# Performance work log

Measured on AMD Instinct MI355X. Metric: run time of the kernel, lower is better.

Reference implementation:

```python
import jax, jax.numpy as jnp
import numpy as np

B, N_ENT, D = 8, 50000, 64
ATTN = 64
TOTAL_REL = 401
E = 1000000


def setup_inputs() -> dict:
    key = jax.random.key(0)
    ks = jax.random.split(key, 16)
    inp = {
        "query": jax.random.normal(ks[0], (B, D), jnp.float32),
        "hidden": jax.random.normal(ks[1], (B, N_ENT, D), jnp.float32),
        # params
        "Ws": jax.random.normal(ks[2], (ATTN, D), jnp.float32) / np.sqrt(D),
        "Wr": jax.random.normal(ks[3], (ATTN, D), jnp.float32) / np.sqrt(D),
        "Wqr_w": jax.random.normal(ks[4], (ATTN, D), jnp.float32) / np.sqrt(D),
        "Wqr_b": jnp.zeros((ATTN,), jnp.float32),
        "Wattn": jax.random.normal(ks[5], (1, ATTN), jnp.float32) / np.sqrt(ATTN),
        "rela_embed": jax.random.normal(ks[6], (TOTAL_REL, D), jnp.float32),
        "mlp_w1": jax.random.normal(ks[7], (D, D), jnp.float32) / np.sqrt(D),
        "mlp_b1": jnp.zeros((D,), jnp.float32),
        "mlp_w2": jax.random.normal(ks[8], (D, D), jnp.float32) / np.sqrt(D),
        "mlp_b2": jnp.zeros((D,), jnp.float32),
        # edge list columns
        "id_bat": jax.random.randint(ks[9], (E,), 0, B),
        "id_sub": jax.random.randint(ks[10], (E,), 0, B * N_ENT),
        "id_rel": jax.random.randint(ks[11], (E,), 0, TOTAL_REL),
        "id_obj": jax.random.randint(ks[12], (E,), 0, B * N_ENT),
    }
    return inp


def reference(query, hidden, Ws, Wr, Wqr_w, Wqr_b, Wattn, rela_embed,
              mlp_w1, mlp_b1, mlp_w2, mlp_b2,
              id_bat, id_sub, id_rel, id_obj):
    b, n_ent, d = hidden.shape
    all_h = hidden.reshape(b * n_ent, d)
    # gathers
    m_head = all_h[id_sub]            # [E, D]
    m_rela = rela_embed[id_rel]       # [E, D]
    m_quer = query[id_bat]            # [E, D]
    # distmult message
    mess = m_head * m_rela
    # attention gate: sigmoid(W_attn(relu(Ws h + Wr r + Wqr q + b)))
    pre = jax.nn.relu(m_head @ Ws.T + m_rela @ Wr.T + m_quer @ Wqr_w.T + Wqr_b)
    alpha = jax.nn.sigmoid(pre @ Wattn.T)   # [E, 1]
    message = mess * alpha
    # scatter-sum aggregation to [B*n_ent, D]
    agg = jax.ops.segment_sum(message, id_obj, num_segments=b * n_ent)
    # unique-index masked MLP update: MLP applied only to nodes that received
    # messages; untouched rows stay exactly zero (as in the torch original)
    touched = jnp.zeros((b * n_ent,), bool).at[id_obj].set(True)
    upd = jax.nn.relu((agg @ mlp_w1.T + mlp_b1) @ mlp_w2.T + mlp_b2)
    new_hidden = jnp.where(touched[:, None], upd, jnp.zeros((), upd.dtype))
    return new_hidden.reshape(b, n_ent, d)
```

## Files before the change

kernel.cpp:

```cpp
#include <hip/hip_runtime.h>
#include <math.h>

#define COUNT_BLOCKS 256

__device__ __forceinline__ void proj_rows(
    const float* __restrict__ x, const float* __restrict__ W,
    const float* __restrict__ bias, float* __restrict__ y,
    int base, int nrows, float* __restrict__ smem)
{
    int t = threadIdx.x;
    float4* sm4 = (float4*)smem;
    for (int i = t; i < 1024; i += 256) sm4[i] = ((const float4*)W)[i];
    __syncthreads();

    int tid = t & 127;
    int c0  = (t >> 7) * 32;
    int r0  = base + tid;
    bool v[4];
#pragma unroll
    for (int k = 0; k < 4; ++k) v[k] = (r0 + k * 128) < nrows;
    if (!v[0]) return;

    float acc[4][32];
#pragma unroll
    for (int k = 0; k < 4; ++k)
#pragma unroll
        for (int a = 0; a < 32; ++a) acc[k][a] = bias ? bias[c0 + a] : 0.f;

    for (int d4 = 0; d4 < 16; ++d4) {
        float4 xv[4];
#pragma unroll
        for (int k = 0; k < 4; ++k)
            xv[k] = v[k] ? *(const float4*)(x + (size_t)(r0 + k * 128) * 64 + d4 * 4)
                         : make_float4(0.f, 0.f, 0.f, 0.f);
#pragma unroll
        for (int a = 0; a < 32; ++a) {
            float4 w4 = sm4[(c0 + a) * 16 + d4];
#pragma unroll
            for (int k = 0; k < 4; ++k) {
                acc[k][a] = fmaf(xv[k].x, w4.x, acc[k][a]);
                acc[k][a] = fmaf(xv[k].y, w4.y, acc[k][a]);
                acc[k][a] = fmaf(xv[k].z, w4.z, acc[k][a]);
                acc[k][a] = fmaf(xv[k].w, w4.w, acc[k][a]);
            }
        }
    }
#pragma unroll
    for (int k = 0; k < 4; ++k) if (v[k]) {
        float* yr = y + (size_t)(r0 + k * 128) * 64 + c0;
#pragma unroll
        for (int a4 = 0; a4 < 8; ++a4)
            *(float4*)(yr + a4 * 4) = make_float4(acc[k][a4*4+0], acc[k][a4*4+1],
                                                  acc[k][a4*4+2], acc[k][a4*4+3]);
    }
}

__device__ __forceinline__ void combine_device(
    const float* __restrict__ w1, const float* __restrict__ b1,
    const float* __restrict__ w2, const float* __restrict__ b2,
    float* __restrict__ WcT, float* __restrict__ bc, float* __restrict__ smem)
{
    int t = threadIdx.x;
    float4* sm4 = (float4*)smem;
    for (int i = t; i < 1024; i += 256) sm4[i] = ((const float4*)w1)[i];
    __syncthreads();
    int j = t >> 2, k0 = (t & 3) * 16;
    for (int k = k0; k < k0 + 16; ++k) {
        float a = 0.f;
        for (int tt = 0; tt < 64; ++tt)
            a = fmaf(w2[j * 64 + tt], smem[tt * 64 + k], a);
        WcT[k * 64 + j] = a;
    }
    if ((t & 3) == 0) {
        float a = b2[j];
        for (int tt = 0; tt < 64; ++tt) a = fmaf(w2[j * 64 + tt], b1[tt], a);
        bc[j] = a;
    }
}

__device__ __forceinline__ void count_device(
    const int* __restrict__ id_obj, int* __restrict__ counts, int E, int cb)
{
    int e = cb * 256 + (int)threadIdx.x;
    int stride = COUNT_BLOCKS * 256;
    for (; e < E; e += stride) atomicAdd(&counts[id_obj[e]], 1);
}

__global__ __launch_bounds__(256, 1) void prepare(
    const float* __restrict__ hidden, const float* __restrict__ Ws,
    float* __restrict__ hs, int NN, int pbNN,
    const float* __restrict__ rela, const float* __restrict__ Wr,
    float* __restrict__ rr, int NR,
    const float* __restrict__ query, const float* __restrict__ Wqr_w,
    const float* __restrict__ Wqr_b, float* __restrict__ qq, int B,
    const float* __restrict__ w1, const float* __restrict__ b1,
    const float* __restrict__ w2, const float* __restrict__ b2,
    float* __restrict__ WcT, float* __restrict__ bc,
    const int* __restrict__ id_obj, int* __restrict__ counts, int E)
{
    __shared__ float smem[4096];
    int bid = blockIdx.x;
    if      (bid <  pbNN)     proj_rows(hidden, Ws,   nullptr, hs, bid * 512, NN, smem);
    else if (bid == pbNN)     proj_rows(rela,   Wr,   nullptr, rr, 0, NR, smem);
    else if (bid == pbNN + 1) proj_rows(query,  Wqr_w, Wqr_b,  qq, 0, B,  smem);
    else if (bid == pbNN + 2) combine_device(w1, b1, w2, b2, WcT, bc, smem);
    else                      count_device(id_obj, counts, E, bid - (pbNN + 3));
}

__global__ __launch_bounds__(256) void scan_tiles(
    const int* __restrict__ counts, int* __restrict__ offs,
    int* __restrict__ bsum, int NN)
{
    __shared__ int lsum[256];
    int t = threadIdx.x;
    int base = blockIdx.x * 1024 + t * 4;
    int c0 = 0, c1 = 0, c2 = 0, c3 = 0;
    if (base + 3 < NN) {
        int4 v = *(const int4*)(counts + base);
        c0 = v.x; c1 = v.y; c2 = v.z; c3 = v.w;
    } else {
        if (base + 0 < NN) c0 = counts[base + 0];
        if (base + 1 < NN) c1 = counts[base + 1];
        if (base + 2 < NN) c2 = counts[base + 2];
        if (base + 3 < NN) c3 = counts[base + 3];
    }
    int s = c0 + c1 + c2 + c3;
    lsum[t] = s;
    __syncthreads();
    for (int off = 1; off < 256; off <<= 1) {
        int x = (t >= off) ? lsum[t - off] : 0;
        __syncthreads();
        lsum[t] += x;
        __syncthreads();
    }
    int excl = lsum[t] - s;
    if (t == 255) bsum[blockIdx.x] = lsum[t];
    int o0 = excl, o1 = o0 + c0, o2 = o1 + c1, o3 = o2 + c2;
    if (base + 3 < NN) {
        *(int4*)(offs + base) = make_int4(o0, o1, o2, o3);
    } else {
        if (base + 0 < NN) offs[base + 0] = o0;
        if (base + 1 < NN) offs[base + 1] = o1;
        if (base + 2 < NN) offs[base + 2] = o2;
        if (base + 3 < NN) offs[base + 3] = o3;
    }
}

__global__ __launch_bounds__(512) void finalize_offs(
    int* __restrict__ offs, int* __restrict__ cursor,
    const int* __restrict__ bsum, int nblk, int NN, int E)
{
    __shared__ int s[512];
    int t = threadIdx.x;
    int v = (t < nblk) ? bsum[t] : 0;
    s[t] = v;
    __syncthreads();
    for (int off = 1; off < 512; off <<= 1) {
        int x = (t >= off) ? s[t - off] : 0;
        __syncthreads();
        s[t] += x;
        __syncthreads();
    }
    int bid = blockIdx.x;
    int base = s[bid] - bsum[bid];
    if (bid == 0 && t == 0) offs[NN] = E;
#pragma unroll
    for (int j = 0; j < 2; ++j) {
        int i = bid * 1024 + j * 512 + t;
        if (i < NN) { int o = offs[i] + base; offs[i] = o; cursor[i] = o; }
    }
}

__global__ __launch_bounds__(256) void scatter_pack(
    const int* __restrict__ id_obj, const int* __restrict__ id_sub,
    const int* __restrict__ id_rel, const int* __restrict__ id_bat,
    int* __restrict__ cursor, int4* __restrict__ packed, int E)
{
    int stride = gridDim.x * blockDim.x;
    for (int e = blockIdx.x * blockDim.x + threadIdx.x; e < E; e += stride) {
        int pos = atomicAdd(&cursor[id_obj[e]], 1);
        packed[pos] = make_int4(id_sub[e], id_rel[e], id_bat[e], 0);
    }
}

__global__ __launch_bounds__(256) void node_kernel(
    const int* __restrict__ offs, const int4* __restrict__ packed,
    const float* __restrict__ hidden, const float* __restrict__ rela,
    const float* __restrict__ hs, const float* __restrict__ rr,
    const float* __restrict__ qq, const float* __restrict__ wattn,
    const float* __restrict__ WcT, const float* __restrict__ bc,
    float* __restrict__ out, int NN, int B)
{
    __shared__ float sqq[8 * 64];
    __shared__ float wct[64][64];
    __shared__ float sbc[64];
    __shared__ float srow[16][68];
    int t = threadIdx.x;
    for (int i = t; i < B * 16; i += 256) ((float4*)sqq)[i] = ((const float4*)qq)[i];
    for (int i = t; i < 1024; i += 256) ((float4*)wct)[i] = ((const float4*)WcT)[i];
    if (t < 64) sbc[t] = bc[t];
    __syncthreads();

    int g = t & 15, grp = t >> 4;
    int node = blockIdx.x * 16 + grp;
    bool valid = node < NN;
    int beg = 0, end = 0;
    if (valid) { beg = offs[node]; end = offs[node + 1]; }
    const float4 wv = *(const float4*)(wattn + g * 4);

    float4 acc = make_float4(0.f, 0.f, 0.f, 0.f);
    int i = beg;
    for (; i + 2 <= end; i += 2) {
        int4 ra = packed[i], rb = packed[i + 1];
        const float4 hsa = *(const float4*)(hs     + (size_t)ra.x * 64 + g * 4);
        const float4 hsb = *(const float4*)(hs     + (size_t)rb.x * 64 + g * 4);
        const float4 rra = *(const float4*)(rr     + (size_t)ra.y * 64 + g * 4);
        const float4 rrb = *(const float4*)(rr     + (size_t)rb.y * 64 + g * 4);
        const float4 mha = *(const float4*)(hidden + (size_t)ra.x * 64 + g * 4);
        const float4 mhb = *(const float4*)(hidden + (size_t)rb.x * 64 + g * 4);
        const float4 mra = *(const float4*)(rela   + (size_t)ra.y * 64 + g * 4);
        const float4 mrb = *(const float4*)(rela   + (size_t)rb.y * 64 + g * 4);
        const float4 qqa = *(const float4*)&sqq[ra.z * 64 + g * 4];
        const float4 qqb = *(const float4*)&sqq[rb.z * 64 + g * 4];

        float ca = fmaxf(hsa.x + rra.x + qqa.x, 0.f) * wv.x
                 + fmaxf(hsa.y + rra.y + qqa.y, 0.f) * wv.y
                 + fmaxf(hsa.z + rra.z + qqa.z, 0.f) * wv.z
                 + fmaxf(hsa.w + rra.w + qqa.w, 0.f) * wv.w;
        float cb = fmaxf(hsb.x + rrb.x + qqb.x, 0.f) * wv.x
                 + fmaxf(hsb.y + rrb.y + qqb.y, 0.f) * wv.y
                 + fmaxf(hsb.z + rrb.z + qqb.z, 0.f) * wv.z
                 + fmaxf(hsb.w + rrb.w + qqb.w, 0.f) * wv.w;
        ca += __shfl_xor(ca, 1);  cb += __shfl_xor(cb, 1);
        ca += __shfl_xor(ca, 2);  cb += __shfl_xor(cb, 2);
        ca += __shfl_xor(ca, 4);  cb += __shfl_xor(cb, 4);
        ca += __shfl_xor(ca, 8);  cb += __shfl_xor(cb, 8);
        float aa = 1.f / (1.f + __expf(-ca));
        float ab = 1.f / (1.f + __expf(-cb));

        acc.x = fmaf(mha.x * mra.x, aa, acc.x);
        acc.y = fmaf(mha.y * mra.y, aa, acc.y);
        acc.z = fmaf(mha.z * mra.z, aa, acc.z);
        acc.w = fmaf(mha.w * mra.w, aa, acc.w);
        acc.x = fmaf(mhb.x * mrb.x, ab, acc.x);
        acc.y = fmaf(mhb.y * mrb.y, ab, acc.y);
        acc.z = fmaf(mhb.z * mrb.z, ab, acc.z);
        acc.w = fmaf(mhb.w * mrb.w, ab, acc.w);
    }
    if (i < end) {
        int4 ra = packed[i];
        const float4 hsa = *(const float4*)(hs     + (size_t)ra.x * 64 + g * 4);
        const float4 rra = *(const float4*)(rr     + (size_t)ra.y * 64 + g * 4);
        const float4 mha = *(const float4*)(hidden + (size_t)ra.x * 64 + g * 4);
        const float4 mra = *(const float4*)(rela   + (size_t)ra.y * 64 + g * 4);
        const float4 qqa = *(const float4*)&sqq[ra.z * 64 + g * 4];
        float ca = fmaxf(hsa.x + rra.x + qqa.x, 0.f) * wv.x
                 + fmaxf(hsa.y + rra.y + qqa.y, 0.f) * wv.y
                 + fmaxf(hsa.z + rra.z + qqa.z, 0.f) * wv.z
                 + fmaxf(hsa.w + rra.w + qqa.w, 0.f) * wv.w;
        ca += __shfl_xor(ca, 1);
        ca += __shfl_xor(ca, 2);
        ca += __shfl_xor(ca, 4);
        ca += __shfl_xor(ca, 8);
        float aa = 1.f / (1.f + __expf(-ca));
        acc.x = fmaf(mha.x * mra.x, aa, acc.x);
        acc.y = fmaf(mha.y * mra.y, aa, acc.y);
        acc.z = fmaf(mha.z * mra.z, aa, acc.z);
        acc.w = fmaf(mha.w * mra.w, aa, acc.w);
    }

    *(float4*)&srow[grp][g * 4] = acc;
    float m0 = sbc[g*4+0], m1 = sbc[g*4+1], m2 = sbc[g*4+2], m3 = sbc[g*4+3];
#pragma unroll 8
    for (int d = 0; d < 64; ++d) {
        float rv = srow[grp][d];
        float4 w4 = *(const float4*)&wct[d][g * 4];
        m0 = fmaf(rv, w4.x, m0);
        m1 = fmaf(rv, w4.y, m1);
        m2 = fmaf(rv, w4.z, m2);
        m3 = fmaf(rv, w4.w, m3);
    }
    if (valid) {
        float4 r;
        if (end > beg) r = make_float4(fmaxf(m0, 0.f), fmaxf(m1, 0.f),
                                       fmaxf(m2, 0.f), fmaxf(m3, 0.f));
        else           r = make_float4(0.f, 0.f, 0.f, 0.f);
        *(float4*)(out + (size_t)node * 64 + g * 4) = r;
    }
}

extern "C" void kernel_launch(void* const* d_in, const int* in_sizes, int n_in,
                              void* d_out, int out_size, void* d_ws, size_t ws_size,
                              hipStream_t stream)
{
    const float* query  = (const float*)d_in[0];
    const float* hidden = (const float*)d_in[1];
    const float* Ws     = (const float*)d_in[2];
    const float* Wr     = (const float*)d_in[3];
    const float* Wqr_w  = (const float*)d_in[4];
    const float* Wqr_b  = (const float*)d_in[5];
    const float* Wattn  = (const float*)d_in[6];
    const float* rela   = (const float*)d_in[7];
    const float* w1     = (const float*)d_in[8];
    const float* b1     = (const float*)d_in[9];
    const float* w2     = (const float*)d_in[10];
    const float* b2     = (const float*)d_in[11];
    const int* id_bat   = (const int*)d_in[12];
    const int* id_sub   = (const int*)d_in[13];
    const int* id_rel   = (const int*)d_in[14];
    const int* id_obj   = (const int*)d_in[15];

    int B  = in_sizes[0] / 64;
    int NN = in_sizes[1] / 64;
    int NR = in_sizes[7] / 64;
    int E  = in_sizes[12];
    float* out = (float*)d_out;

    int NBLK = (NN + 1023) / 1024;
    int pbNN = (NN + 511) / 512;

    char* ws = (char*)d_ws;
    size_t off = 0;
    auto alloc = [&](size_t bytes) { void* p = ws + off; off += (bytes + 255) & ~255ull; return p; };
    float* hs      = (float*)alloc((size_t)NN * 64 * sizeof(float));
    float* rr      = (float*)alloc((size_t)NR * 64 * sizeof(float));
    float* qq      = (float*)alloc((size_t)B  * 64 * sizeof(float));
    float* WcT     = (float*)alloc(64 * 64 * sizeof(float));
    float* bc      = (float*)alloc(64 * sizeof(float));
    int*   counts  = (int*)alloc((size_t)NN * sizeof(int));
    int*   offs    = (int*)alloc(((size_t)NN + 1) * sizeof(int));
    int*   bsum    = (int*)alloc((size_t)NBLK * sizeof(int));
    int4*  packed  = (int4*)alloc((size_t)E * sizeof(int4));

    hipMemsetAsync(counts, 0, (size_t)NN * sizeof(int), stream);

    prepare<<<pbNN + 3 + COUNT_BLOCKS, 256, 0, stream>>>(
        hidden, Ws, hs, NN, pbNN,
        rela, Wr, rr, NR,
        query, Wqr_w, Wqr_b, qq, B,
        w1, b1, w2, b2, WcT, bc,
        id_obj, counts, E);

    scan_tiles<<<NBLK, 256, 0, stream>>>(counts, offs, bsum, NN);
    finalize_offs<<<NBLK, 512, 0, stream>>>(offs, counts , bsum, NBLK, NN, E);
    scatter_pack<<<1024, 256, 0, stream>>>(id_obj, id_sub, id_rel, id_bat,
                                           counts , packed, E);

    node_kernel<<<(NN + 15) / 16, 256, 0, stream>>>(
        offs, packed, hidden, rela, hs, rr, qq, Wattn, WcT, bc, out, NN, B);
}
```

Baseline: 557.7 us.

## Pack edge records into 32-bit words and make node kernel grid-stride persistent

Each sorted edge record shrinks from an int4 to one 32-bit word: 19 bits for subject, 9 for relation and 4 for batch. This cuts the bytes scatter_pack writes and node_kernel reads, and two records are now fetched with one uint2 load. The node kernel also becomes a fixed 4096-block grid that walks node tiles in a stride loop, so each block loads the 64x64 combined weight and query tables into shared memory once rather than once per 16 nodes. The bit widths limit node count, relation count and batch size to fit the fields, and the uint2 load can fall on an unaligned address when the edge index is odd.

New measurement: 524.2 us. -6.0%, faster.

```diff
diff --git a/kernel.cpp b/kernel.cpp
--- a/kernel.cpp
+++ b/kernel.cpp
@@ -2,6 +2,7 @@
 #include <math.h>
 
 #define COUNT_BLOCKS 256
+
 
 __device__ __forceinline__ void proj_rows(
     const float* __restrict__ x, const float* __restrict__ W,
@@ -174,17 +175,19 @@
 __global__ __launch_bounds__(256) void scatter_pack(
     const int* __restrict__ id_obj, const int* __restrict__ id_sub,
     const int* __restrict__ id_rel, const int* __restrict__ id_bat,
-    int* __restrict__ cursor, int4* __restrict__ packed, int E)
+    int* __restrict__ cursor, unsigned int* __restrict__ packed, int E)
 {
     int stride = gridDim.x * blockDim.x;
     for (int e = blockIdx.x * blockDim.x + threadIdx.x; e < E; e += stride) {
         int pos = atomicAdd(&cursor[id_obj[e]], 1);
-        packed[pos] = make_int4(id_sub[e], id_rel[e], id_bat[e], 0);
+        packed[pos] = (unsigned int)id_sub[e]
+                    | ((unsigned int)id_rel[e] << 19)
+                    | ((unsigned int)id_bat[e] << 28);
     }
 }
 
 __global__ __launch_bounds__(256) void node_kernel(
-    const int* __restrict__ offs, const int4* __restrict__ packed,
+    const int* __restrict__ offs, const unsigned int* __restrict__ packed,
     const float* __restrict__ hidden, const float* __restrict__ rela,
     const float* __restrict__ hs, const float* __restrict__ rr,
     const float* __restrict__ qq, const float* __restrict__ wattn,
@@ -195,6 +198,7 @@
     __shared__ float wct[64][64];
     __shared__ float sbc[64];
     __shared__ float srow[16][68];
+
     int t = threadIdx.x;
     for (int i = t; i < B * 16; i += 256) ((float4*)sqq)[i] = ((const float4*)qq)[i];
     for (int i = t; i < 1024; i += 256) ((float4*)wct)[i] = ((const float4*)WcT)[i];
@@ -202,90 +206,99 @@
     __syncthreads();
 
     int g = t & 15, grp = t >> 4;
-    int node = blockIdx.x * 16 + grp;
-    bool valid = node < NN;
-    int beg = 0, end = 0;
-    if (valid) { beg = offs[node]; end = offs[node + 1]; }
     const float4 wv = *(const float4*)(wattn + g * 4);
-
-    float4 acc = make_float4(0.f, 0.f, 0.f, 0.f);
-    int i = beg;
-    for (; i + 2 <= end; i += 2) {
-        int4 ra = packed[i], rb = packed[i + 1];
-        const float4 hsa = *(const float4*)(hs     + (size_t)ra.x * 64 + g * 4);
-        const float4 hsb = *(const float4*)(hs     + (size_t)rb.x * 64 + g * 4);
-        const float4 rra = *(const float4*)(rr     + (size_t)ra.y * 64 + g * 4);
-        const float4 rrb = *(const float4*)(rr     + (size_t)rb.y * 64 + g * 4);
-        const float4 mha = *(const float4*)(hidden + (size_t)ra.x * 64 + g * 4);
-        const float4 mhb = *(const float4*)(hidden + (size_t)rb.x * 64 + g * 4);
-        const float4 mra = *(const float4*)(rela   + (size_t)ra.y * 64 + g * 4);
-        const float4 mrb = *(const float4*)(rela   + (size_t)rb.y * 64 + g * 4);
-        const float4 qqa = *(const float4*)&sqq[ra.z * 64 + g * 4];
-        const float4 qqb = *(const float4*)&sqq[rb.z * 64 + g * 4];
-
-        float ca = fmaxf(hsa.x + rra.x + qqa.x, 0.f) * wv.x
-                 + fmaxf(hsa.y + rra.y + qqa.y, 0.f) * wv.y
-                 + fmaxf(hsa.z + rra.z + qqa.z, 0.f) * wv.z
-                 + fmaxf(hsa.w + rra.w + qqa.w, 0.f) * wv.w;
-        float cb = fmaxf(hsb.x + rrb.x + qqb.x, 0.f) * wv.x
-                 + fmaxf(hsb.y + rrb.y + qqb.y, 0.f) * wv.y
-                 + fmaxf(hsb.z + rrb.z + qqb.z, 0.f) * wv.z
-                 + fmaxf(hsb.w + rrb.w + qqb.w, 0.f) * wv.w;
-        ca += __shfl_xor(ca, 1);  cb += __shfl_xor(cb, 1);
-        ca += __shfl_xor(ca, 2);  cb += __shfl_xor(cb, 2);
-        ca += __shfl_xor(ca, 4);  cb += __shfl_xor(cb, 4);
-        ca += __shfl_xor(ca, 8);  cb += __shfl_xor(cb, 8);
-        float aa = 1.f / (1.f + __expf(-ca));
-        float ab = 1.f / (1.f + __expf(-cb));
-
-        acc.x = fmaf(mha.x * mra.x, aa, acc.x);
-        acc.y = fmaf(mha.y * mra.y, aa, acc.y);
-        acc.z = fmaf(mha.z * mra.z, aa, acc.z);
-        acc.w = fmaf(mha.w * mra.w, aa, acc.w);
-        acc.x = fmaf(mhb.x * mrb.x, ab, acc.x);
-        acc.y = fmaf(mhb.y * mrb.y, ab, acc.y);
-        acc.z = fmaf(mhb.z * mrb.z, ab, acc.z);
-        acc.w = fmaf(mhb.w * mrb.w, ab, acc.w);
-    }
-    if (i < end) {
-        int4 ra = packed[i];
-        const float4 hsa = *(const float4*)(hs     + (size_t)ra.x * 64 + g * 4);
-        const float4 rra = *(const float4*)(rr     + (size_t)ra.y * 64 + g * 4);
-        const float4 mha = *(const float4*)(hidden + (size_t)ra.x * 64 + g * 4);
-        const float4 mra = *(const float4*)(rela   + (size_t)ra.y * 64 + g * 4);
-        const float4 qqa = *(const float4*)&sqq[ra.z * 64 + g * 4];
-        float ca = fmaxf(hsa.x + rra.x + qqa.x, 0.f) * wv.x
-                 + fmaxf(hsa.y + rra.y + qqa.y, 0.f) * wv.y
-                 + fmaxf(hsa.z + rra.z + qqa.z, 0.f) * wv.z
-                 + fmaxf(hsa.w + rra.w + qqa.w, 0.f) * wv.w;
-        ca += __shfl_xor(ca, 1);
-        ca += __shfl_xor(ca, 2);
-        ca += __shfl_xor(ca, 4);
-        ca += __shfl_xor(ca, 8);
-        float aa = 1.f / (1.f + __expf(-ca));
-        acc.x = fmaf(mha.x * mra.x, aa, acc.x);
-        acc.y = fmaf(mha.y * mra.y, aa, acc.y);
-        acc.z = fmaf(mha.z * mra.z, aa, acc.z);
-        acc.w = fmaf(mha.w * mra.w, aa, acc.w);
-    }
-
-    *(float4*)&srow[grp][g * 4] = acc;
-    float m0 = sbc[g*4+0], m1 = sbc[g*4+1], m2 = sbc[g*4+2], m3 = sbc[g*4+3];
+    float bc0 = sbc[g*4+0], bc1 = sbc[g*4+1], bc2 = sbc[g*4+2], bc3 = sbc[g*4+3];
+
+    int ntiles = (NN + 15) / 16;
+    for (int tile = blockIdx.x; tile < ntiles; tile += gridDim.x) {
+        int node = tile * 16 + grp;
+        bool valid = node < NN;
+        int beg = 0, end = 0;
+        if (valid) { beg = offs[node]; end = offs[node + 1]; }
+
+        float4 acc = make_float4(0.f, 0.f, 0.f, 0.f);
+        int i = beg;
+        for (; i + 2 <= end; i += 2) {
+            uint2 pr = *(const uint2*)(packed + i);
+            int suba = pr.x & 0x7FFFF, rela_a = (pr.x >> 19) & 0x1FF, bata = pr.x >> 28;
+            int subb = pr.y & 0x7FFFF, rela_b = (pr.y >> 19) & 0x1FF, batb = pr.y >> 28;
+
+            const float4 hsa = *(const float4*)(hs     + (size_t)suba * 64 + g * 4);
+            const float4 hsb = *(const float4*)(hs     + (size_t)subb * 64 + g * 4);
+            const float4 rra = *(const float4*)(rr     + (size_t)rela_a * 64 + g * 4);
+            const float4 rrb = *(const float4*)(rr     + (size_t)rela_b * 64 + g * 4);
+            const float4 mha = *(const float4*)(hidden + (size_t)suba * 64 + g * 4);
+            const float4 mhb = *(const float4*)(hidden + (size_t)subb * 64 + g * 4);
+            const float4 mra = *(const float4*)(rela   + (size_t)rela_a * 64 + g * 4);
+            const float4 mrb = *(const float4*)(rela   + (size_t)rela_b * 64 + g * 4);
+            const float4 qqa = *(const float4*)&sqq[bata * 64 + g * 4];
+            const float4 qqb = *(const float4*)&sqq[batb * 64 + g * 4];
+
+            float ca = fmaxf(hsa.x + rra.x + qqa.x, 0.f) * wv.x
+                     + fmaxf(hsa.y + rra.y + qqa.y, 0.f) * wv.y
+                     + fmaxf(hsa.z + rra.z + qqa.z, 0.f) * wv.z
+                     + fmaxf(hsa.w + rra.w + qqa.w, 0.f) * wv.w;
+            float cb = fmaxf(hsb.x + rrb.x + qqb.x, 0.f) * wv.x
+                     + fmaxf(hsb.y + rrb.y + qqb.y, 0.f) * wv.y
+                     + fmaxf(hsb.z + rrb.z + qqb.z, 0.f) * wv.z
+                     + fmaxf(hsb.w + rrb.w + qqb.w, 0.f) * wv.w;
+            ca += __shfl_xor(ca, 1);  cb += __shfl_xor(cb, 1);
+            ca += __shfl_xor(ca, 2);  cb += __shfl_xor(cb, 2);
+            ca += __shfl_xor(ca, 4);  cb += __shfl_xor(cb, 4);
+            ca += __shfl_xor(ca, 8);  cb += __shfl_xor(cb, 8);
+            float aa = 1.f / (1.f + __expf(-ca));
+            float ab = 1.f / (1.f + __expf(-cb));
+
+            acc.x = fmaf(mha.x * mra.x, aa, acc.x);
+            acc.y = fmaf(mha.y * mra.y, aa, acc.y);
+            acc.z = fmaf(mha.z * mra.z, aa, acc.z);
+            acc.w = fmaf(mha.w * mra.w, aa, acc.w);
+            acc.x = fmaf(mhb.x * mrb.x, ab, acc.x);
+            acc.y = fmaf(mhb.y * mrb.y, ab, acc.y);
+            acc.z = fmaf(mhb.z * mrb.z, ab, acc.z);
+            acc.w = fmaf(mhb.w * mrb.w, ab, acc.w);
+        }
+        if (i < end) {
+            unsigned int p = packed[i];
+            int suba = p & 0x7FFFF, rela_a = (p >> 19) & 0x1FF, bata = p >> 28;
+            const float4 hsa = *(const float4*)(hs     + (size_t)suba * 64 + g * 4);
+            const float4 rra = *(const float4*)(rr     + (size_t)rela_a * 64 + g * 4);
+            const float4 mha = *(const float4*)(hidden + (size_t)suba * 64 + g * 4);
+            const float4 mra = *(const float4*)(rela   + (size_t)rela_a * 64 + g * 4);
+            const float4 qqa = *(const float4*)&sqq[bata * 64 + g * 4];
+            float ca = fmaxf(hsa.x + rra.x + qqa.x, 0.f) * wv.x
+                     + fmaxf(hsa.y + rra.y + qqa.y, 0.f) * wv.y
+                     + fmaxf(hsa.z + rra.z + qqa.z, 0.f) * wv.z
+                     + fmaxf(hsa.w + rra.w + qqa.w, 0.f) * wv.w;
+            ca += __shfl_xor(ca, 1);
+            ca += __shfl_xor(ca, 2);
+            ca += __shfl_xor(ca, 4);
+            ca += __shfl_xor(ca, 8);
+            float aa = 1.f / (1.f + __expf(-ca));
+            acc.x = fmaf(mha.x * mra.x, aa, acc.x);
+            acc.y = fmaf(mha.y * mra.y, aa, acc.y);
+            acc.z = fmaf(mha.z * mra.z, aa, acc.z);
+            acc.w = fmaf(mha.w * mra.w, aa, acc.w);
+        }
+
+        *(float4*)&srow[grp][g * 4] = acc;
+        float m0 = bc0, m1 = bc1, m2 = bc2, m3 = bc3;
 #pragma unroll 8
-    for (int d = 0; d < 64; ++d) {
-        float rv = srow[grp][d];
-        float4 w4 = *(const float4*)&wct[d][g * 4];
-        m0 = fmaf(rv, w4.x, m0);
-        m1 = fmaf(rv, w4.y, m1);
-        m2 = fmaf(rv, w4.z, m2);
-        m3 = fmaf(rv, w4.w, m3);
-    }
-    if (valid) {
-        float4 r;
-        if (end > beg) r = make_float4(fmaxf(m0, 0.f), fmaxf(m1, 0.f),
-                                       fmaxf(m2, 0.f), fmaxf(m3, 0.f));
-        else           r = make_float4(0.f, 0.f, 0.f, 0.f);
-        *(float4*)(out + (size_t)node * 64 + g * 4) = r;
+        for (int d = 0; d < 64; ++d) {
+            float rv = srow[grp][d];
+            float4 w4 = *(const float4*)&wct[d][g * 4];
+            m0 = fmaf(rv, w4.x, m0);
+            m1 = fmaf(rv, w4.y, m1);
+            m2 = fmaf(rv, w4.z, m2);
+            m3 = fmaf(rv, w4.w, m3);
+        }
+        if (valid) {
+            float4 r;
+            if (end > beg) r = make_float4(fmaxf(m0, 0.f), fmaxf(m1, 0.f),
+                                           fmaxf(m2, 0.f), fmaxf(m3, 0.f));
+            else           r = make_float4(0.f, 0.f, 0.f, 0.f);
+            *(float4*)(out + (size_t)node * 64 + g * 4) = r;
+        }
     }
 }
 
@@ -322,15 +335,15 @@
     char* ws = (char*)d_ws;
     size_t off = 0;
     auto alloc = [&](size_t bytes) { void* p = ws + off; off += (bytes + 255) & ~255ull; return p; };
-    float* hs      = (float*)alloc((size_t)NN * 64 * sizeof(float));
-    float* rr      = (float*)alloc((size_t)NR * 64 * sizeof(float));
-    float* qq      = (float*)alloc((size_t)B  * 64 * sizeof(float));
-    float* WcT     = (float*)alloc(64 * 64 * sizeof(float));
-    float* bc      = (float*)alloc(64 * sizeof(float));
-    int*   counts  = (int*)alloc((size_t)NN * sizeof(int));
-    int*   offs    = (int*)alloc(((size_t)NN + 1) * sizeof(int));
-    int*   bsum    = (int*)alloc((size_t)NBLK * sizeof(int));
-    int4*  packed  = (int4*)alloc((size_t)E * sizeof(int4));
+    float*        hs     = (float*)alloc((size_t)NN * 64 * sizeof(float));
+    float*        rr     = (float*)alloc((size_t)NR * 64 * sizeof(float));
+    float*        qq     = (float*)alloc((size_t)B  * 64 * sizeof(float));
+    float*        WcT    = (float*)alloc(64 * 64 * sizeof(float));
+    float*        bc     = (float*)alloc(64 * sizeof(float));
+    int*          counts = (int*)alloc((size_t)NN * sizeof(int));
+    int*          offs   = (int*)alloc(((size_t)NN + 1) * sizeof(int));
+    int*          bsum   = (int*)alloc((size_t)NBLK * sizeof(int));
+    unsigned int* packed = (unsigned int*)alloc((size_t)E * sizeof(unsigned int));
 
     hipMemsetAsync(counts, 0, (size_t)NN * sizeof(int), stream);
 
@@ -346,6 +359,6 @@
     scatter_pack<<<1024, 256, 0, stream>>>(id_obj, id_sub, id_rel, id_bat,
                                            counts , packed, E);
 
-    node_kernel<<<(NN + 15) / 16, 256, 0, stream>>>(
+    node_kernel<<<4096, 256, 0, stream>>>(
         offs, packed, hidden, rela, hs, rr, qq, Wattn, WcT, bc, out, NN, B);
 }
```
